# Kernel tuning notes

Hardware: AMD Instinct MI355X
Metric: run time of the kernel (lower is better)

The kernel has to match this reference:

```python
import jax, jax.numpy as jnp
import numpy as np

IN, H, FC1, FC2, OUT = 3, 30, 64, 32, 1
B, T = 8192, 256


def _lstm_layer(xT, W_ih, W_hh, b_ih, b_hh):
    """xT: (T, B, Din). Returns (hidden sequence (T,B,H), final h (B,H)).
    PyTorch gate order: i, f, g, o."""
    # Precompute input contribution for all timesteps (one big GEMM).
    gx = jnp.einsum('tbd,gd->tbg', xT, W_ih) + b_ih + b_hh  # (T,B,4H)
    b = xT.shape[1]
    h0 = jnp.zeros((b, W_hh.shape[1]), xT.dtype)
    c0 = h0

    def step(carry, g):
        h, c = carry
        gates = g + h @ W_hh.T
        i, f, gg, o = jnp.split(gates, 4, axis=-1)
        i = jax.nn.sigmoid(i)
        f = jax.nn.sigmoid(f)
        gg = jnp.tanh(gg)
        o = jax.nn.sigmoid(o)
        c = f * c + i * gg
        h = o * jnp.tanh(c)
        return (h, c), h

    (h_n, _), ys = jax.lax.scan(step, (h0, c0), gx)
    return ys, h_n


def setup_inputs() -> dict:
    key = jax.random.key(0)
    ks = jax.random.split(key, 16)
    s = 0.18  # ~1/sqrt(hidden_size), matches PyTorch uniform init scale
    inp = {
        'x': jax.random.normal(ks[0], (B, T, IN), jnp.float32),
        'W_ih0': jax.random.normal(ks[1], (4 * H, IN), jnp.float32) * s,
        'W_hh0': jax.random.normal(ks[2], (4 * H, H), jnp.float32) * s,
        'b_ih0': jax.random.normal(ks[3], (4 * H,), jnp.float32) * s,
        'b_hh0': jax.random.normal(ks[4], (4 * H,), jnp.float32) * s,
        'W_ih1': jax.random.normal(ks[5], (4 * H, H), jnp.float32) * s,
        'W_hh1': jax.random.normal(ks[6], (4 * H, H), jnp.float32) * s,
        'b_ih1': jax.random.normal(ks[7], (4 * H,), jnp.float32) * s,
        'b_hh1': jax.random.normal(ks[8], (4 * H,), jnp.float32) * s,
        'W_fc1': jax.random.normal(ks[9], (FC1, H), jnp.float32) * s,
        'b_fc1': jax.random.normal(ks[10], (FC1,), jnp.float32) * s,
        'W_fc2': jax.random.normal(ks[11], (FC2, FC1), jnp.float32) * 0.125,
        'b_fc2': jax.random.normal(ks[12], (FC2,), jnp.float32) * 0.125,
        'W_fc3': jax.random.normal(ks[13], (OUT, FC2), jnp.float32) * 0.17,
        'b_fc3': jax.random.normal(ks[14], (OUT,), jnp.float32) * 0.17,
    }
    return inp


def reference(x, W_ih0, W_hh0, b_ih0, b_hh0, W_ih1, W_hh1, b_ih1, b_hh1,
              W_fc1, b_fc1, W_fc2, b_fc2, W_fc3, b_fc3):
    xT = jnp.swapaxes(x, 0, 1)  # (T,B,IN)
    ys, _ = _lstm_layer(xT, W_ih0, W_hh0, b_ih0, b_hh0)   # layer 0 sequence
    _, h_n = _lstm_layer(ys, W_ih1, W_hh1, b_ih1, b_hh1)  # layer 1 final h
    # FC head (dropout = identity in eval mode)
    z = jax.nn.relu(h_n @ W_fc1.T + b_fc1)
    z = jax.nn.relu(z @ W_fc2.T + b_fc2)
    z = jax.nn.sigmoid(z @ W_fc3.T + b_fc3)
    return z.squeeze(-1)  # (B,)
```

## Files before the change

kernel.cpp:

```cpp
#include <hip/hip_runtime.h>

#define TT   256
#define HID  30
#define LOG2E 1.4426950408889634f
#define HS   56

typedef __bf16 bf16x8_t __attribute__((ext_vector_type(8)));
typedef float  f32x4_t  __attribute__((ext_vector_type(4)));

__device__ __forceinline__ float fexp2(float x){
#if __has_builtin(__builtin_amdgcn_exp2f)
    return __builtin_amdgcn_exp2f(x);
#else
    return exp2f(x);
#endif
}
__device__ __forceinline__ float frcp(float x){
#if __has_builtin(__builtin_amdgcn_rcpf)
    return __builtin_amdgcn_rcpf(x);
#else
    return 1.f/x;
#endif
}
__device__ __forceinline__ float fsigmoid(float x){ return frcp(1.f + fexp2(-LOG2E*x)); }
__device__ __forceinline__ float ftanh_f(float x){ return 2.f*frcp(1.f + fexp2(-2.f*LOG2E*x)) - 1.f; }
__device__ __forceinline__ f32x4_t exp4(f32x4_t v){
    f32x4_t e; e[0]=fexp2(v[0]); e[1]=fexp2(v[1]); e[2]=fexp2(v[2]); e[3]=fexp2(v[3]); return e;
}
__device__ __forceinline__ f32x4_t rcp4(f32x4_t v){
    f32x4_t r; r[0]=frcp(v[0]); r[1]=frcp(v[1]); r[2]=frcp(v[2]); r[3]=frcp(v[3]); return r;
}

__global__ __launch_bounds__(512, 4)
void lstm_fused(const float* __restrict__ x,
    const float* __restrict__ Wih0, const float* __restrict__ Whh0,
    const float* __restrict__ bih0, const float* __restrict__ bhh0,
    const float* __restrict__ Wih1, const float* __restrict__ Whh1,
    const float* __restrict__ bih1, const float* __restrict__ bhh1,
    const float* __restrict__ Wfc1, const float* __restrict__ bfc1,
    const float* __restrict__ Wfc2, const float* __restrict__ bfc2,
    const float* __restrict__ Wfc3, const float* __restrict__ bfc3,
    float* __restrict__ out)
{
    __shared__ __align__(16) __bf16 h0f[2][16][HS];
    __shared__ __align__(16) __bf16 h1f[2][16][HS];
    __shared__ float h1_last[16*32];
    __shared__ float zbuf[16*64];
    __shared__ float z2buf[16*32];

    const int tid  = threadIdx.x;
    const int lane = tid & 63;
    const int wvf  = tid >> 6;
    const bool grpA = (wvf < 4);
    const int wv   = wvf & 3;
    const int n    = lane & 15;
    const int q    = lane >> 4;
    const int nl   = n & 7;
    const int u    = wv*8 + nl;
    const int hi   = n >> 3;
    const bool colok = (u < HID);
    const int bbase = blockIdx.x * 16;

    const int uq  = colok ? u : 0;
    const int wr0 = (hi ? 1 : 0)*HID + uq;
    const int wr1 = (hi ? 3 : 2)*HID + uq;

    bf16x8_t fbA{}, fbB{}, fbC{}, fbD{};
    float b0=0.f, b1=0.f, wx20=0.f, wx21=0.f;
    if (grpA) {
        #pragma unroll
        for (int j = 0; j < 8; ++j) {
            int k = q*8 + j;
            float v0=0.f, v1=0.f;
            if (colok) {
                if (k < HID) { v0 = Whh0[wr0*HID+k];      v1 = Whh0[wr1*HID+k]; }
                else         { v0 = Wih0[wr0*3+(k-HID)];  v1 = Wih0[wr1*3+(k-HID)]; }
            }
            fbA[j]=(__bf16)v0; fbB[j]=(__bf16)v1;
        }
        if (colok) {
            b0 = bih0[wr0] + bhh0[wr0];
            b1 = bih0[wr1] + bhh0[wr1];
            wx20 = Wih0[wr0*3+2];  wx21 = Wih0[wr1*3+2];
        }
    } else {
        #pragma unroll
        for (int j = 0; j < 8; ++j) {
            int k = q*8 + j;
            float v0=0.f, v1=0.f, v2=0.f, v3=0.f;
            if (colok && k < HID) {
                v0 = Wih1[wr0*HID+k];  v1 = Wih1[wr1*HID+k];
                v2 = Whh1[wr0*HID+k];  v3 = Whh1[wr1*HID+k];
            }
            fbA[j]=(__bf16)v0; fbB[j]=(__bf16)v1;
            fbC[j]=(__bf16)v2; fbD[j]=(__bf16)v3;
        }
        if (colok) {
            b0 = bih1[wr0] + bhh1[wr0];
            b1 = bih1[wr1] + bhh1[wr1];
        }
    }
    const f32x4_t bv0 = {b0,b0,b0,b0};
    const f32x4_t bv1 = {b1,b1,b1,b1};
    const float mco1 = (hi==0) ? (-2.f*LOG2E) : (-LOG2E);
    const float aco1 = (hi==0) ? 2.f : 1.f;
    const float bco1 = (hi==0) ? -1.f : 0.f;

    f32x4_t cst = {0.f,0.f,0.f,0.f};

    for (int i = tid; i < 2*16*HS; i += 512) {
        (&h0f[0][0][0])[i] = (__bf16)0.f;
        (&h1f[0][0][0])[i] = (__bf16)0.f;
    }
    __syncthreads();
    if (tid < 32) {
        int m = tid >> 1, cc = tid & 1;
        h0f[1][m][30+cc] = (__bf16)x[(size_t)(bbase+m)*(TT*3) + cc];
    }
    __syncthreads();

    const float* xB = x + (size_t)bbase*(TT*3);
    const int xo2  = (q*4)*(TT*3) + 2;
    const int xo01 = (tid>>1)*(TT*3) + (tid&1);
    f32x4_t x2 = {0.f,0.f,0.f,0.f};
    if (grpA) {
        x2[0]=xB[xo2]; x2[1]=xB[xo2+TT*3]; x2[2]=xB[xo2+2*TT*3]; x2[3]=xB[xo2+3*TT*3];
    }

#define STEP(S, RB, WB, FIRST) do {                                            \
    if (grpA) {                                                                \
        bf16x8_t A0 = *(const bf16x8_t*)(&h0f[RB][n][q*8]);                    \
        f32x4_t bx0 = bv0 + x2*wx20;                                           \
        f32x4_t bx1 = bv1 + x2*wx21;                                           \
        f32x4_t a0 = __builtin_amdgcn_mfma_f32_16x16x32_bf16(A0, fbA, bx0, 0,0,0); \
        f32x4_t a1 = __builtin_amdgcn_mfma_f32_16x16x32_bf16(A0, fbB, bx1, 0,0,0); \
        const int tpre = ((S)+2 < TT) ? (S)+2 : TT-1;                          \
        const float* xs = xB + 3*tpre;                                         \
        f32x4_t x2n;                                                           \
        x2n[0]=xs[xo2]; x2n[1]=xs[xo2+TT*3];                                   \
        x2n[2]=xs[xo2+2*TT*3]; x2n[3]=xs[xo2+3*TT*3];                          \
        float x01v = 0.f;                                                      \
        if (tid < 32) x01v = xs[xo01];                                         \
        f32x4_t g0 = rcp4(exp4(a0*(-LOG2E)) + 1.f);                            \
        f32x4_t g1 = rcp4(exp4(a1*mco1) + 1.f)*aco1 + bco1;                    \
        f32x4_t p  = g0*g1;                                                    \
        p[0]=__shfl_xor(p[0],8,64); p[1]=__shfl_xor(p[1],8,64);                \
        p[2]=__shfl_xor(p[2],8,64); p[3]=__shfl_xor(p[3],8,64);                \
        cst = g0*cst + p;                                                      \
        float cA=cst[0], oA=g1[0], cB=cst[1], oB=g1[1];                        \
        float c2=__shfl_xor(cst[2],8,64), c3=__shfl_xor(cst[3],8,64);          \
        float o2=__shfl_xor(g1[2],8,64),  o3=__shfl_xor(g1[3],8,64);           \
        if (!hi) { cA=c2; oA=o2; cB=c3; oB=o3; }                               \
        float hA = oA*ftanh_f(cA);                                             \
        float hB = oB*ftanh_f(cB);                                             \
        const int row = q*4 + (hi ? 0 : 2);                                    \
        if (colok) {                                                           \
            h0f[WB][row][u]   = (__bf16)hA;                                    \
            h0f[WB][row+1][u] = (__bf16)hB;                                    \
        }                                                                      \
        if (tid < 32) h0f[WB][tid>>1][30+(tid&1)] = (__bf16)x01v;              \
        x2 = x2n;                                                              \
    } else if (!(FIRST)) {                                                     \
        bf16x8_t A1 = *(const bf16x8_t*)(&h0f[RB][n][q*8]);                    \
        bf16x8_t A2 = *(const bf16x8_t*)(&h1f[RB][n][q*8]);                    \
        f32x4_t d0 = __builtin_amdgcn_mfma_f32_16x16x32_bf16(A2, fbC, bv0, 0,0,0); \
        d0         = __builtin_amdgcn_mfma_f32_16x16x32_bf16(A1, fbA, d0,  0,0,0); \
        f32x4_t d1 = __builtin_amdgcn_mfma_f32_16x16x32_bf16(A2, fbD, bv1, 0,0,0); \
        d1         = __builtin_amdgcn_mfma_f32_16x16x32_bf16(A1, fbB, d1,  0,0,0); \
        f32x4_t g0 = rcp4(exp4(d0*(-LOG2E)) + 1.f);                            \
        f32x4_t g1 = rcp4(exp4(d1*mco1) + 1.f)*aco1 + bco1;                    \
        f32x4_t p  = g0*g1;                                                    \
        p[0]=__shfl_xor(p[0],8,64); p[1]=__shfl_xor(p[1],8,64);                \
        p[2]=__shfl_xor(p[2],8,64); p[3]=__shfl_xor(p[3],8,64);                \
        cst = g0*cst + p;                                                      \
        float cA=cst[0], oA=g1[0], cB=cst[1], oB=g1[1];                        \
        float c2=__shfl_xor(cst[2],8,64), c3=__shfl_xor(cst[3],8,64);          \
        float o2=__shfl_xor(g1[2],8,64),  o3=__shfl_xor(g1[3],8,64);           \
        if (!hi) { cA=c2; oA=o2; cB=c3; oB=o3; }                               \
        float hA = oA*ftanh_f(cA);                                             \
        float hB = oB*ftanh_f(cB);                                             \
        const int row = q*4 + (hi ? 0 : 2);                                    \
        if (colok) {                                                           \
            h1f[WB][row][u]   = (__bf16)hA;                                    \
            h1f[WB][row+1][u] = (__bf16)hB;                                    \
            if ((S) == TT-1) {                                                 \
                h1_last[row*32+u]     = hA;                                    \
                h1_last[(row+1)*32+u] = hB;                                    \
            }                                                                  \
        }                                                                      \
    }                                                                          \
    __syncthreads();                                                           \
} while (0)

    STEP(-1, 1, 0, 1);
    #pragma unroll 1
    for (int s = 0; s < TT; s += 2) {
        STEP(s,   0, 1, 0);
        STEP(s+1, 1, 0, 0);
    }
#undef STEP

    #pragma unroll
    for (int rep = 0; rep < 2; ++rep) {
        int idx = tid + rep*512;
        int m = idx >> 6, uu = idx & 63;
        float a = bfc1[uu];
        for (int k = 0; k < HID; ++k) a += h1_last[m*32+k] * Wfc1[uu*HID+k];
        zbuf[m*64+uu] = fmaxf(a, 0.f);
    }
    __syncthreads();
    {
        int m = tid >> 5, v = tid & 31;
        float a = bfc2[v];
        for (int k = 0; k < 64; ++k) a += zbuf[m*64+k] * Wfc2[v*64+k];
        z2buf[m*32+v] = fmaxf(a, 0.f);
    }
    __syncthreads();
    if (tid < 16) {
        float a = bfc3[0];
        for (int k = 0; k < 32; ++k) a += z2buf[tid*32+k] * Wfc3[k];
        out[bbase + tid] = fsigmoid(a);
    }
}

extern "C" void kernel_launch(void* const* d_in, const int* in_sizes, int n_in,
                              void* d_out, int out_size, void* d_ws, size_t ws_size,
                              hipStream_t stream) {
    const float* x    = (const float*)d_in[0];
    const float* Wih0 = (const float*)d_in[1];
    const float* Whh0 = (const float*)d_in[2];
    const float* bih0 = (const float*)d_in[3];
    const float* bhh0 = (const float*)d_in[4];
    const float* Wih1 = (const float*)d_in[5];
    const float* Whh1 = (const float*)d_in[6];
    const float* bih1 = (const float*)d_in[7];
    const float* bhh1 = (const float*)d_in[8];
    const float* Wfc1 = (const float*)d_in[9];
    const float* bfc1 = (const float*)d_in[10];
    const float* Wfc2 = (const float*)d_in[11];
    const float* bfc2 = (const float*)d_in[12];
    const float* Wfc3 = (const float*)d_in[13];
    const float* bfc3 = (const float*)d_in[14];
    float* outp = (float*)d_out;

    hipLaunchKernelGGL(lstm_fused, dim3(512), dim3(512), 0, stream,
        x, Wih0, Whh0, bih0, bhh0, Wih1, Whh1, bih1, bhh1,
        Wfc1, bfc1, Wfc2, bfc2, Wfc3, bfc3, outp);
}
```

Before: 329.9 us.

## Process two independent 16-row batch tiles per block to interleave recurrences

Each block now handles 32 batch rows as two independent 16-row sub-tiles. Every wave runs two LSTM recurrences per timestep, so their MFMA and transcendental latencies can overlap, and the cost of each per-step __syncthreads is shared across twice the work. Grid size halves to 256 blocks and launch bounds drop to 2 blocks per CU. This trades fewer resident blocks and higher register pressure for more instruction-level parallelism within each wave.

```diff
diff --git a/kernel.cpp b/kernel.cpp
--- a/kernel.cpp
+++ b/kernel.cpp
@@ -4,6 +4,7 @@
 #define HID  30
 #define LOG2E 1.4426950408889634f
 #define HS   56
+#define XROW (TT*3)
 
 typedef __bf16 bf16x8_t __attribute__((ext_vector_type(8)));
 typedef float  f32x4_t  __attribute__((ext_vector_type(4)));
@@ -31,7 +32,9 @@
     f32x4_t r; r[0]=frcp(v[0]); r[1]=frcp(v[1]); r[2]=frcp(v[2]); r[3]=frcp(v[3]); return r;
 }
 
-__global__ __launch_bounds__(512, 4)
+#define MFMA(A,B,C) __builtin_amdgcn_mfma_f32_16x16x32_bf16(A,B,C,0,0,0)
+
+__global__ __launch_bounds__(512, 2)
 void lstm_fused(const float* __restrict__ x,
     const float* __restrict__ Wih0, const float* __restrict__ Whh0,
     const float* __restrict__ bih0, const float* __restrict__ bhh0,
@@ -42,11 +45,11 @@
     const float* __restrict__ Wfc3, const float* __restrict__ bfc3,
     float* __restrict__ out)
 {
-    __shared__ __align__(16) __bf16 h0f[2][16][HS];
-    __shared__ __align__(16) __bf16 h1f[2][16][HS];
-    __shared__ float h1_last[16*32];
-    __shared__ float zbuf[16*64];
-    __shared__ float z2buf[16*32];
+    __shared__ __align__(16) __bf16 h0f[2][2][16][HS];
+    __shared__ __align__(16) __bf16 h1f[2][2][16][HS];
+    __shared__ float h1_last[32*32];
+    __shared__ float zbuf[32*64];
+    __shared__ float z2buf[32*32];
 
     const int tid  = threadIdx.x;
     const int lane = tid & 63;
@@ -59,7 +62,7 @@
     const int u    = wv*8 + nl;
     const int hi   = n >> 3;
     const bool colok = (u < HID);
-    const int bbase = blockIdx.x * 16;
+    const int bbase = blockIdx.x * 32;
 
     const int uq  = colok ? u : 0;
     const int wr0 = (hi ? 1 : 0)*HID + uq;
@@ -106,88 +109,105 @@
     const float aco1 = (hi==0) ? 2.f : 1.f;
     const float bco1 = (hi==0) ? -1.f : 0.f;
 
-    f32x4_t cst = {0.f,0.f,0.f,0.f};
-
-    for (int i = tid; i < 2*16*HS; i += 512) {
-        (&h0f[0][0][0])[i] = (__bf16)0.f;
-        (&h1f[0][0][0])[i] = (__bf16)0.f;
-    }
-    __syncthreads();
-    if (tid < 32) {
+    f32x4_t cst[2] = {{0.f,0.f,0.f,0.f},{0.f,0.f,0.f,0.f}};
+
+    for (int i = tid; i < 2*2*16*HS; i += 512) {
+        (&h0f[0][0][0][0])[i] = (__bf16)0.f;
+        (&h1f[0][0][0][0])[i] = (__bf16)0.f;
+    }
+    __syncthreads();
+    if (tid < 64) {
         int m = tid >> 1, cc = tid & 1;
-        h0f[1][m][30+cc] = (__bf16)x[(size_t)(bbase+m)*(TT*3) + cc];
-    }
-    __syncthreads();
-
-    const float* xB = x + (size_t)bbase*(TT*3);
-    const int xo2  = (q*4)*(TT*3) + 2;
-    const int xo01 = (tid>>1)*(TT*3) + (tid&1);
-    f32x4_t x2 = {0.f,0.f,0.f,0.f};
+        h0f[m>>4][1][m&15][30+cc] = (__bf16)x[(size_t)(bbase+m)*XROW + cc];
+    }
+    __syncthreads();
+
+    const float* xB = x + (size_t)bbase*XROW;
+    const int xo2  = (q*4)*XROW + 2;
+    const int xo01 = (tid>>1)*XROW + (tid&1);
+    f32x4_t x2[2] = {{0.f,0.f,0.f,0.f},{0.f,0.f,0.f,0.f}};
     if (grpA) {
-        x2[0]=xB[xo2]; x2[1]=xB[xo2+TT*3]; x2[2]=xB[xo2+2*TT*3]; x2[3]=xB[xo2+3*TT*3];
-    }
-
-#define STEP(S, RB, WB, FIRST) do {                                            \
+        #pragma unroll
+        for (int r=0;r<4;++r){
+            x2[0][r] = xB[xo2 + r*XROW];
+            x2[1][r] = xB[16*XROW + xo2 + r*XROW];
+        }
+    }
+
+#define L0S(ST, RB, WB) { \
+    bf16x8_t A0 = *(const bf16x8_t*)(&h0f[ST][RB][n][q*8]); \
+    f32x4_t a0 = MFMA(A0, fbA, bv0 + x2[ST]*wx20); \
+    f32x4_t a1 = MFMA(A0, fbB, bv1 + x2[ST]*wx21); \
+    f32x4_t g0 = rcp4(exp4(a0*(-LOG2E)) + 1.f); \
+    f32x4_t g1 = rcp4(exp4(a1*mco1) + 1.f)*aco1 + bco1; \
+    f32x4_t p  = g0*g1; \
+    p[0]=__shfl_xor(p[0],8,64); p[1]=__shfl_xor(p[1],8,64); \
+    p[2]=__shfl_xor(p[2],8,64); p[3]=__shfl_xor(p[3],8,64); \
+    cst[ST] = g0*cst[ST] + p; \
+    float cA=cst[ST][0], oA=g1[0], cB=cst[ST][1], oB=g1[1]; \
+    float c2=__shfl_xor(cst[ST][2],8,64), c3=__shfl_xor(cst[ST][3],8,64); \
+    float o2=__shfl_xor(g1[2],8,64),  o3=__shfl_xor(g1[3],8,64); \
+    if (!hi) { cA=c2; oA=o2; cB=c3; oB=o3; } \
+    float hA = oA*ftanh_f(cA); \
+    float hB = oB*ftanh_f(cB); \
+    const int row = q*4 + (hi ? 0 : 2); \
+    if (colok) { \
+        h0f[ST][WB][row][u]   = (__bf16)hA; \
+        h0f[ST][WB][row+1][u] = (__bf16)hB; \
+    } \
+}
+
+#define L1S(ST, SS, RB, WB) { \
+    bf16x8_t A1 = *(const bf16x8_t*)(&h0f[ST][RB][n][q*8]); \
+    bf16x8_t A2 = *(const bf16x8_t*)(&h1f[ST][RB][n][q*8]); \
+    f32x4_t d0 = MFMA(A2, fbC, bv0); d0 = MFMA(A1, fbA, d0); \
+    f32x4_t d1 = MFMA(A2, fbD, bv1); d1 = MFMA(A1, fbB, d1); \
+    f32x4_t g0 = rcp4(exp4(d0*(-LOG2E)) + 1.f); \
+    f32x4_t g1 = rcp4(exp4(d1*mco1) + 1.f)*aco1 + bco1; \
+    f32x4_t p  = g0*g1; \
+    p[0]=__shfl_xor(p[0],8,64); p[1]=__shfl_xor(p[1],8,64); \
+    p[2]=__shfl_xor(p[2],8,64); p[3]=__shfl_xor(p[3],8,64); \
+    cst[ST] = g0*cst[ST] + p; \
+    float cA=cst[ST][0], oA=g1[0], cB=cst[ST][1], oB=g1[1]; \
+    float c2=__shfl_xor(cst[ST][2],8,64), c3=__shfl_xor(cst[ST][3],8,64); \
+    float o2=__shfl_xor(g1[2],8,64),  o3=__shfl_xor(g1[3],8,64); \
+    if (!hi) { cA=c2; oA=o2; cB=c3; oB=o3; } \
+    float hA = oA*ftanh_f(cA); \
+    float hB = oB*ftanh_f(cB); \
+    const int row = q*4 + (hi ? 0 : 2); \
+    if (colok) { \
+        h1f[ST][WB][row][u]   = (__bf16)hA; \
+        h1f[ST][WB][row+1][u] = (__bf16)hB; \
+        if ((SS) == TT-1) { \
+            h1_last[((ST)*16+row)*32+u]   = hA; \
+            h1_last[((ST)*16+row+1)*32+u] = hB; \
+        } \
+    } \
+}
+
+#define STEP(SS, RB, WB, FIRST) do {                                           \
     if (grpA) {                                                                \
-        bf16x8_t A0 = *(const bf16x8_t*)(&h0f[RB][n][q*8]);                    \
-        f32x4_t bx0 = bv0 + x2*wx20;                                           \
-        f32x4_t bx1 = bv1 + x2*wx21;                                           \
-        f32x4_t a0 = __builtin_amdgcn_mfma_f32_16x16x32_bf16(A0, fbA, bx0, 0,0,0); \
-        f32x4_t a1 = __builtin_amdgcn_mfma_f32_16x16x32_bf16(A0, fbB, bx1, 0,0,0); \
-        const int tpre = ((S)+2 < TT) ? (S)+2 : TT-1;                          \
+                     \
+        const int tpre = ((SS)+2 < TT) ? (SS)+2 : TT-1;                        \
         const float* xs = xB + 3*tpre;                                         \
-        f32x4_t x2n;                                                           \
-        x2n[0]=xs[xo2]; x2n[1]=xs[xo2+TT*3];                                   \
-        x2n[2]=xs[xo2+2*TT*3]; x2n[3]=xs[xo2+3*TT*3];                          \
+        f32x4_t xnX, xnY;                                                      \
+        _Pragma("unroll")                                                      \
+        for (int r=0;r<4;++r){                                                 \
+            xnX[r] = xs[xo2 + r*XROW];                                         \
+            xnY[r] = xs[16*XROW + xo2 + r*XROW];                               \
+        }                                                                      \
         float x01v = 0.f;                                                      \
-        if (tid < 32) x01v = xs[xo01];                                         \
-        f32x4_t g0 = rcp4(exp4(a0*(-LOG2E)) + 1.f);                            \
-        f32x4_t g1 = rcp4(exp4(a1*mco1) + 1.f)*aco1 + bco1;                    \
-        f32x4_t p  = g0*g1;                                                    \
-        p[0]=__shfl_xor(p[0],8,64); p[1]=__shfl_xor(p[1],8,64);                \
-        p[2]=__shfl_xor(p[2],8,64); p[3]=__shfl_xor(p[3],8,64);                \
-        cst = g0*cst + p;                                                      \
-        float cA=cst[0], oA=g1[0], cB=cst[1], oB=g1[1];                        \
-        float c2=__shfl_xor(cst[2],8,64), c3=__shfl_xor(cst[3],8,64);          \
-        float o2=__shfl_xor(g1[2],8,64),  o3=__shfl_xor(g1[3],8,64);           \
-        if (!hi) { cA=c2; oA=o2; cB=c3; oB=o3; }                               \
-        float hA = oA*ftanh_f(cA);                                             \
-        float hB = oB*ftanh_f(cB);                                             \
-        const int row = q*4 + (hi ? 0 : 2);                                    \
-        if (colok) {                                                           \
-            h0f[WB][row][u]   = (__bf16)hA;                                    \
-            h0f[WB][row+1][u] = (__bf16)hB;                                    \
+        if (tid < 64) x01v = xs[xo01];                                         \
+        L0S(0, RB, WB)                                                         \
+        L0S(1, RB, WB)                                                         \
+        if (tid < 64) {                                                        \
+            int m = tid >> 1;                                                  \
+            h0f[m>>4][WB][m&15][30+(tid&1)] = (__bf16)x01v;                    \
         }                                                                      \
-        if (tid < 32) h0f[WB][tid>>1][30+(tid&1)] = (__bf16)x01v;              \
-        x2 = x2n;                                                              \
+        x2[0] = xnX;  x2[1] = xnY;                                             \
     } else if (!(FIRST)) {                                                     \
-        bf16x8_t A1 = *(const bf16x8_t*)(&h0f[RB][n][q*8]);                    \
-        bf16x8_t A2 = *(const bf16x8_t*)(&h1f[RB][n][q*8]);                    \
-        f32x4_t d0 = __builtin_amdgcn_mfma_f32_16x16x32_bf16(A2, fbC, bv0, 0,0,0); \
-        d0         = __builtin_amdgcn_mfma_f32_16x16x32_bf16(A1, fbA, d0,  0,0,0); \
-        f32x4_t d1 = __builtin_amdgcn_mfma_f32_16x16x32_bf16(A2, fbD, bv1, 0,0,0); \
-        d1         = __builtin_amdgcn_mfma_f32_16x16x32_bf16(A1, fbB, d1,  0,0,0); \
-        f32x4_t g0 = rcp4(exp4(d0*(-LOG2E)) + 1.f);                            \
-        f32x4_t g1 = rcp4(exp4(d1*mco1) + 1.f)*aco1 + bco1;                    \
-        f32x4_t p  = g0*g1;                                                    \
-        p[0]=__shfl_xor(p[0],8,64); p[1]=__shfl_xor(p[1],8,64);                \
-        p[2]=__shfl_xor(p[2],8,64); p[3]=__shfl_xor(p[3],8,64);                \
-        cst = g0*cst + p;                                                      \
-        float cA=cst[0], oA=g1[0], cB=cst[1], oB=g1[1];                        \
-        float c2=__shfl_xor(cst[2],8,64), c3=__shfl_xor(cst[3],8,64);          \
-        float o2=__shfl_xor(g1[2],8,64),  o3=__shfl_xor(g1[3],8,64);           \
-        if (!hi) { cA=c2; oA=o2; cB=c3; oB=o3; }                               \
-        float hA = oA*ftanh_f(cA);                                             \
-        float hB = oB*ftanh_f(cB);                                             \
-        const int row = q*4 + (hi ? 0 : 2);                                    \
-        if (colok) {                                                           \
-            h1f[WB][row][u]   = (__bf16)hA;                                    \
-            h1f[WB][row+1][u] = (__bf16)hB;                                    \
-            if ((S) == TT-1) {                                                 \
-                h1_last[row*32+u]     = hA;                                    \
-                h1_last[(row+1)*32+u] = hB;                                    \
-            }                                                                  \
-        }                                                                      \
+        L1S(0, SS, RB, WB)                                                     \
+        L1S(1, SS, RB, WB)                                                     \
     }                                                                          \
     __syncthreads();                                                           \
 } while (0)
@@ -199,9 +219,11 @@
         STEP(s+1, 1, 0, 0);
     }
 #undef STEP
+#undef L0S
+#undef L1S
 
     #pragma unroll
-    for (int rep = 0; rep < 2; ++rep) {
+    for (int rep = 0; rep < 4; ++rep) {
         int idx = tid + rep*512;
         int m = idx >> 6, uu = idx & 63;
         float a = bfc1[uu];
@@ -209,14 +231,16 @@
         zbuf[m*64+uu] = fmaxf(a, 0.f);
     }
     __syncthreads();
-    {
-        int m = tid >> 5, v = tid & 31;
+    #pragma unroll
+    for (int rep = 0; rep < 2; ++rep) {
+        int idx = tid + rep*512;
+        int m = idx >> 5, v = idx & 31;
         float a = bfc2[v];
         for (int k = 0; k < 64; ++k) a += zbuf[m*64+k] * Wfc2[v*64+k];
         z2buf[m*32+v] = fmaxf(a, 0.f);
     }
     __syncthreads();
-    if (tid < 16) {
+    if (tid < 32) {
         float a = bfc3[0];
         for (int k = 0; k < 32; ++k) a += z2buf[tid*32+k] * Wfc3[k];
         out[bbase + tid] = fsigmoid(a);
@@ -243,7 +267,7 @@
     const float* bfc3 = (const float*)d_in[14];
     float* outp = (float*)d_out;
 
-    hipLaunchKernelGGL(lstm_fused, dim3(512), dim3(512), 0, stream,
+    hipLaunchKernelGGL(lstm_fused, dim3(256), dim3(512), 0, stream,
         x, Wih0, Whh0, bih0, bhh0, Wih1, Whh1, bih1, bhh1,
         Wfc1, bfc1, Wfc2, bfc2, Wfc3, bfc3, outp);
 }
```

New measurement: 356.7 us. +8.1%, slower.
